# Performance work log

Hardware: AMD Instinct MI355X
Metric: run time of the kernel (lower is better)

Reference implementation:

```python
import jax, jax.numpy as jnp
import numpy as np

N_NODES = 50000
N_EDGES = 1600000
IN_DIM, HID_DIM, OUT_DIM, HEADS = 128, 128, 64, 8
NEG_SLOPE = 0.2
BN_EPS = 1e-5


def setup_inputs() -> dict:
    key = jax.random.key(0)
    ks = jax.random.split(key, 12)
    hpc = HID_DIM // HEADS  # per-head channels of layer 1
    return {
        "x": jax.random.normal(ks[0], (N_NODES, IN_DIM), jnp.float32),
        "edge_index": jax.random.randint(ks[1], (2, N_EDGES), 0, N_NODES, jnp.int64),
        "W1": jax.random.normal(ks[2], (IN_DIM, HEADS * hpc), jnp.float32) * 0.05,
        "a1_src": jax.random.normal(ks[3], (HEADS, hpc), jnp.float32) * 0.1,
        "a1_dst": jax.random.normal(ks[4], (HEADS, hpc), jnp.float32) * 0.1,
        "b1": jnp.zeros((HEADS * hpc,), jnp.float32),
        "bn_gamma": jnp.ones((HID_DIM,), jnp.float32),
        "bn_beta": jnp.zeros((HID_DIM,), jnp.float32),
        "W2": jax.random.normal(ks[5], (HID_DIM, OUT_DIM), jnp.float32) * 0.05,
        "a2_src": jax.random.normal(ks[6], (1, OUT_DIM), jnp.float32) * 0.1,
        "a2_dst": jax.random.normal(ks[7], (1, OUT_DIM), jnp.float32) * 0.1,
        "b2": jnp.zeros((OUT_DIM,), jnp.float32),
    }


def _gat_conv(x, src, dst, W, a_src, a_dst, bias, heads, n_nodes):
    # x: [N, Fin]; src/dst: [E'] (self-loops already appended)
    hpc = W.shape[1] // heads
    h = (x @ W).reshape(n_nodes, heads, hpc)                 # [N,H,C]
    alpha_s = jnp.einsum("nhc,hc->nh", h, a_src)             # [N,H]
    alpha_d = jnp.einsum("nhc,hc->nh", h, a_dst)
    e = alpha_s[src] + alpha_d[dst]                          # [E',H]
    e = jax.nn.leaky_relu(e, NEG_SLOPE)
    # segment softmax over destination neighborhoods
    m = jax.ops.segment_max(e, dst, num_segments=n_nodes)    # [N,H]
    m = jnp.where(jnp.isfinite(m), m, 0.0)
    ee = jnp.exp(e - m[dst])
    denom = jax.ops.segment_sum(ee, dst, num_segments=n_nodes)
    alpha = ee / (denom[dst] + 1e-16)                        # [E',H]
    msg = h[src] * alpha[:, :, None]                         # [E',H,C]
    out = jax.ops.segment_sum(msg, dst, num_segments=n_nodes)  # [N,H,C]
    return out.reshape(n_nodes, heads * hpc) + bias


def _batch_norm(x, gamma, beta):
    mu = jnp.mean(x, axis=0)
    var = jnp.var(x, axis=0)
    return gamma * (x - mu) * jax.lax.rsqrt(var + BN_EPS) + beta


def reference(x, edge_index, W1, a1_src, a1_dst, b1, bn_gamma, bn_beta, W2, a2_src, a2_dst, b2):
    n = x.shape[0]
    loops = jnp.arange(n, dtype=edge_index.dtype)
    src = jnp.concatenate([edge_index[0], loops])            # PyG add_self_loops
    dst = jnp.concatenate([edge_index[1], loops])
    h = _gat_conv(x, src, dst, W1, a1_src, a1_dst, b1, HEADS, n)
    h = _batch_norm(h, bn_gamma, bn_beta)
    h = jax.nn.elu(h)
    # dropout: identity at inference
    out = _gat_conv(h, src, dst, W2, a2_src, a2_dst, b2, 1, n)
    return out
```

## Files before the change

### kernel.cpp

```cpp
#include <hip/hip_runtime.h>
#include <hip/hip_bf16.h>

#define N_NODES 50000
#define N_EDGES 1600000
#define HEADS 8
#define NBK 196
#define NBLK 196

typedef unsigned short u16;
typedef unsigned int u32;

__device__ __forceinline__ float bf2f(u16 u) {
  union { u32 i; float f; } v; v.i = ((u32)u) << 16; return v.f;
}
__device__ __forceinline__ float bflo(u32 p) {
  union { u32 i; float f; } v; v.i = p << 16; return v.f;
}
__device__ __forceinline__ float bfhi(u32 p) {
  union { u32 i; float f; } v; v.i = p & 0xffff0000u; return v.f;
}
__device__ __forceinline__ u16 f2bf(float f) {
  union { float f; u32 i; } v; v.f = f;
  u32 r = v.i + 0x7fff + ((v.i >> 16) & 1);
  return (u16)(r >> 16);
}
__device__ __forceinline__ u32 pack2(float a, float b) {
  return (u32)f2bf(a) | ((u32)f2bf(b) << 16);
}

__global__ void k_detect(const u16* __restrict__ x, const u32* __restrict__ ei,
                         int* __restrict__ flags) {
  __shared__ int cbig, cnz;
  if (threadIdx.x == 0) { cbig = 0; cnz = 0; }
  __syncthreads();
  int lb = 0, ln = 0;
  for (int i = threadIdx.x; i < 4096; i += 256) {
    int ex = (x[i] >> 7) & 0xff;
    lb += (ex >= 140);
    if (i < 2048) ln += (ei[2 * i + 1] != 0);
  }
  atomicAdd(&cbig, lb); atomicAdd(&cnz, ln);
  __syncthreads();
  if (threadIdx.x == 0) {
    flags[0] = (cbig > 16) ? 1 : 0;
    flags[1] = (cnz == 0) ? 1 : 0;
  }
}

__global__ void k_convsmall(const void* a1s, const void* a1d, const void* b1,
                            const void* gam, const void* bet, const void* a2s,
                            const void* a2d, const void* b2, const void* W1,
                            const void* W2, float* __restrict__ outbuf,
                            const int* __restrict__ flags) {
  int i = blockIdx.x * 256 + threadIdx.x;
  if (i >= 25408) return;
  const void* src; int off;
  if (i >= 17216)      { src = W2;  off = i - 17216; }
  else if (i >= 832)   { src = W1;  off = i - 832; }
  else if (i >= 768)   { src = b2;  off = i - 768; }
  else if (i >= 704)   { src = a2d; off = i - 704; }
  else if (i >= 640)   { src = a2s; off = i - 640; }
  else if (i >= 512)   { src = bet; off = i - 512; }
  else if (i >= 384)   { src = gam; off = i - 384; }
  else if (i >= 256)   { src = b1;  off = i - 256; }
  else if (i >= 128)   { src = a1d; off = i - 128; }
  else                 { src = a1s; off = i; }
  outbuf[i] = flags[0] ? ((const float*)src)[off] : bf2f(((const u16*)src)[off]);
}

__global__ __launch_bounds__(256) void k_hist(const int* __restrict__ ei,
                                              int* __restrict__ H,
                                              int* __restrict__ totals,
                                              const int* __restrict__ flags) {
  __shared__ int hist[NBK];
  int t = threadIdx.x, blk = blockIdx.x;
  for (int i = t; i < NBK; i += 256) hist[i] = 0;
  __syncthreads();
  bool i64 = flags[1] != 0;
  int base = blk * 8192;
  for (int k = 0; k < 32; k++) {
    int e = base + k * 256 + t;
    if (e < N_EDGES) {
      int d = i64 ? ei[2 * (N_EDGES + e)] : ei[N_EDGES + e];
      atomicAdd(&hist[d >> 8], 1);
    }
  }
  __syncthreads();
  for (int i = t; i < NBK; i += 256) {
    H[i * NBLK + blk] = hist[i];
    atomicAdd(&totals[i], hist[i]);
  }
}

__global__ void k_scan_tot(const int* __restrict__ totals, int* __restrict__ bucketBase) {
  __shared__ int tmp[256];
  int t = threadIdx.x;
  int v = (t < NBK) ? totals[t] : 0;
  tmp[t] = v; __syncthreads();
  for (int o = 1; o < 256; o <<= 1) {
    int x = (t >= o) ? tmp[t - o] : 0; __syncthreads();
    tmp[t] += x; __syncthreads();
  }
  if (t < NBK) bucketBase[t] = tmp[t] - v;
  if (t == NBK - 1) bucketBase[NBK] = tmp[t];
}

__global__ void k_scan_blk(const int* __restrict__ H, const int* __restrict__ bucketBase,
                           int* __restrict__ P) {
  __shared__ int tmp[256];
  int t = threadIdx.x, b = blockIdx.x;
  int v = (t < NBLK) ? H[b * NBLK + t] : 0;
  tmp[t] = v; __syncthreads();
  for (int o = 1; o < 256; o <<= 1) {
    int x = (t >= o) ? tmp[t - o] : 0; __syncthreads();
    tmp[t] += x; __syncthreads();
  }
  if (t < NBLK) P[b * NBLK + t] = bucketBase[b] + tmp[t] - v;
}

__global__ __launch_bounds__(256) void k_bucket(const int* __restrict__ ei,
                                                const int* __restrict__ P,
                                                u32* __restrict__ buf,
                                                const int* __restrict__ flags) {
  __shared__ int cur[NBK];
  int t = threadIdx.x, blk = blockIdx.x;
  for (int i = t; i < NBK; i += 256) cur[i] = P[i * NBLK + blk];
  __syncthreads();
  bool i64 = flags[1] != 0;
  int base = blk * 8192;
  for (int k = 0; k < 32; k++) {
    int e = base + k * 256 + t;
    if (e < N_EDGES) {
      int s = i64 ? ei[2 * e] : ei[e];
      int d = i64 ? ei[2 * (N_EDGES + e)] : ei[N_EDGES + e];
      int pos = atomicAdd(&cur[d >> 8], 1);
      buf[pos] = ((u32)(d & 255) << 16) | (u32)s;
    }
  }
}

__global__ __launch_bounds__(256) void k_csr(const u32* __restrict__ buf,
                                             const int* __restrict__ bucketBase,
                                             int* __restrict__ row_start,
                                             int* __restrict__ deg,
                                             int* __restrict__ csr, int N) {
  __shared__ int cnt[256], scn[256], cur[256];
  int b = blockIdx.x, t = threadIdx.x;
  int lo = bucketBase[b], hi = bucketBase[b + 1];
  cnt[t] = 0; __syncthreads();
  for (int e = lo + t; e < hi; e += 256) atomicAdd(&cnt[(buf[e] >> 16) & 255], 1);
  __syncthreads();
  int v = cnt[t];
  scn[t] = v; __syncthreads();
  for (int o = 1; o < 256; o <<= 1) {
    int x = (t >= o) ? scn[t - o] : 0; __syncthreads();
    scn[t] += x; __syncthreads();
  }
  int excl = scn[t] - v;
  int node = b * 256 + t;
  if (node < N) { row_start[node] = lo + excl; deg[node] = v; }
  cur[t] = lo + excl;
  __syncthreads();
  for (int e = lo + t; e < hi; e += 256) {
    u32 p = buf[e];
    int d8 = (p >> 16) & 255;
    int pos = atomicAdd(&cur[d8], 1);
    csr[pos] = p & 0xffff;
  }
}

template <bool EPI, bool AFLAG>
__global__ __launch_bounds__(256) void k_gemm(const void* __restrict__ A,
                                              const float* __restrict__ B,
                                              const float* __restrict__ scale,
                                              const float* __restrict__ shift,
                                              u16* __restrict__ C, int M, int ncoltot,
                                              const int* __restrict__ flags) {
  constexpr int K = 128, KP = K + 4;
  __shared__ float As[64 * KP];
  __shared__ float Bs[K * 64];
  int t = threadIdx.x;
  int row0 = blockIdx.x * 64, co = blockIdx.y * 64;
  bool af32 = AFLAG ? (flags[0] != 0) : false;
  for (int i = t; i < K * 16; i += 256) {
    int r = i >> 4, c4 = i & 15;
    ((float4*)Bs)[r * 16 + c4] = ((const float4*)B)[(size_t)r * (ncoltot >> 2) + (co >> 2) + c4];
  }
  for (int i = t; i < 64 * 32; i += 256) {
    int r = i >> 5, c4 = i & 31;
    float4 v = make_float4(0.f, 0.f, 0.f, 0.f);
    int row = row0 + r;
    if (row < M) {
      if (af32) {
        v = ((const float4*)A)[(size_t)row * 32 + c4];
      } else {
        uint2 p = ((const uint2*)A)[(size_t)row * 32 + c4];
        v.x = bflo(p.x); v.y = bfhi(p.x); v.z = bflo(p.y); v.w = bfhi(p.y);
      }
      if (EPI) {
        int c = c4 * 4;
        v.x = fmaf(v.x, scale[c],     shift[c]);     v.x = v.x > 0.f ? v.x : __expf(v.x) - 1.f;
        v.y = fmaf(v.y, scale[c + 1], shift[c + 1]); v.y = v.y > 0.f ? v.y : __expf(v.y) - 1.f;
        v.z = fmaf(v.z, scale[c + 2], shift[c + 2]); v.z = v.z > 0.f ? v.z : __expf(v.z) - 1.f;
        v.w = fmaf(v.w, scale[c + 3], shift[c + 3]); v.w = v.w > 0.f ? v.w : __expf(v.w) - 1.f;
      }
    }
    *(float4*)&As[r * KP + c4 * 4] = v;
  }
  __syncthreads();
  int tx = t & 7, ty = t >> 3;
  int c0 = tx * 8, r0 = ty * 2;
  float acc[2][8];
#pragma unroll
  for (int i = 0; i < 2; i++) for (int j = 0; j < 8; j++) acc[i][j] = 0.f;
#pragma unroll 4
  for (int k = 0; k < K; k++) {
    float4 b0 = *(const float4*)&Bs[k * 64 + c0];
    float4 b1 = *(const float4*)&Bs[k * 64 + c0 + 4];
    float a0 = As[r0 * KP + k];
    float a1 = As[(r0 + 1) * KP + k];
    acc[0][0] = fmaf(a0, b0.x, acc[0][0]); acc[0][1] = fmaf(a0, b0.y, acc[0][1]);
    acc[0][2] = fmaf(a0, b0.z, acc[0][2]); acc[0][3] = fmaf(a0, b0.w, acc[0][3]);
    acc[0][4] = fmaf(a0, b1.x, acc[0][4]); acc[0][5] = fmaf(a0, b1.y, acc[0][5]);
    acc[0][6] = fmaf(a0, b1.z, acc[0][6]); acc[0][7] = fmaf(a0, b1.w, acc[0][7]);
    acc[1][0] = fmaf(a1, b0.x, acc[1][0]); acc[1][1] = fmaf(a1, b0.y, acc[1][1]);
    acc[1][2] = fmaf(a1, b0.z, acc[1][2]); acc[1][3] = fmaf(a1, b0.w, acc[1][3]);
    acc[1][4] = fmaf(a1, b1.x, acc[1][4]); acc[1][5] = fmaf(a1, b1.y, acc[1][5]);
    acc[1][6] = fmaf(a1, b1.z, acc[1][6]); acc[1][7] = fmaf(a1, b1.w, acc[1][7]);
  }
#pragma unroll
  for (int i = 0; i < 2; i++) {
    int row = row0 + r0 + i;
    if (row < M) {
      u32* cp = (u32*)&C[(size_t)row * ncoltot + co + c0];
      cp[0] = pack2(acc[i][0], acc[i][1]);
      cp[1] = pack2(acc[i][2], acc[i][3]);
      cp[2] = pack2(acc[i][4], acc[i][5]);
      cp[3] = pack2(acc[i][6], acc[i][7]);
    }
  }
}

__global__ void k_alpha1(const u16* __restrict__ h1b, const float* __restrict__ a1s,
                         const float* __restrict__ a1d, float* __restrict__ as_out,
                         float* __restrict__ ad_out, int N) {
  int idx = blockIdx.x * 256 + threadIdx.x;
  if (idx >= N * HEADS) return;
  int n = idx >> 3, h = idx & 7;
  const u32* hp = (const u32*)&h1b[((size_t)n << 7) + (h << 4)];
  float s = 0.f, d = 0.f;
#pragma unroll
  for (int q = 0; q < 8; q++) {
    u32 p = hp[q];
    float v0 = bflo(p), v1 = bfhi(p);
    int b = (h << 4) + q * 2;
    s = fmaf(v0, a1s[b], s); s = fmaf(v1, a1s[b + 1], s);
    d = fmaf(v0, a1d[b], d); d = fmaf(v1, a1d[b + 1], d);
  }
  as_out[idx] = s; ad_out[idx] = d;
}

__global__ __launch_bounds__(256) void k_agg1(const u16* __restrict__ h1b,
                                              const float* __restrict__ as_,
                                              const float* __restrict__ ad_,
                                              const int* __restrict__ csr,
                                              const int* __restrict__ row_start,
                                              const int* __restrict__ deg,
                                              const float* __restrict__ b1,
                                              u16* __restrict__ out, int N) {
  int w = threadIdx.x >> 6;
  int node = blockIdx.x * 4 + w;
  if (node >= N) return;
  int l = threadIdx.x & 63;
  int head = l >> 3;
  int st = row_start[node], cnt = deg[node];
  float ad = ad_[(node << 3) | head];
  float s = 0.f, a0 = 0.f, a1 = 0.f;
  const u32* h32 = (const u32*)h1b;
  int j = 0;
  for (; j + 4 <= cnt; j += 4) {
    int s0 = csr[st + j], s1 = csr[st + j + 1], s2 = csr[st + j + 2], s3 = csr[st + j + 3];
    float e0 = as_[(s0 << 3) | head], e1 = as_[(s1 << 3) | head];
    float e2 = as_[(s2 << 3) | head], e3 = as_[(s3 << 3) | head];
    u32 h0 = h32[(s0 << 6) | l], h1v = h32[(s1 << 6) | l];
    u32 h2v = h32[(s2 << 6) | l], h3 = h32[(s3 << 6) | l];
    e0 += ad; e0 = fmaxf(e0, 0.2f * e0); float p0 = __expf(e0);
    e1 += ad; e1 = fmaxf(e1, 0.2f * e1); float p1 = __expf(e1);
    e2 += ad; e2 = fmaxf(e2, 0.2f * e2); float p2 = __expf(e2);
    e3 += ad; e3 = fmaxf(e3, 0.2f * e3); float p3 = __expf(e3);
    s += (p0 + p1) + (p2 + p3);
    a0 = fmaf(p0, bflo(h0), a0);  a1 = fmaf(p0, bfhi(h0), a1);
    a0 = fmaf(p1, bflo(h1v), a0); a1 = fmaf(p1, bfhi(h1v), a1);
    a0 = fmaf(p2, bflo(h2v), a0); a1 = fmaf(p2, bfhi(h2v), a1);
    a0 = fmaf(p3, bflo(h3), a0);  a1 = fmaf(p3, bfhi(h3), a1);
  }
  for (; j < cnt; j++) {
    int s0 = csr[st + j];
    float e0 = as_[(s0 << 3) | head] + ad;
    e0 = fmaxf(e0, 0.2f * e0);
    float p0 = __expf(e0);
    u32 h0 = h32[(s0 << 6) | l];
    s += p0;
    a0 = fmaf(p0, bflo(h0), a0); a1 = fmaf(p0, bfhi(h0), a1);
  }
  {
    float e0 = as_[(node << 3) | head] + ad;
    e0 = fmaxf(e0, 0.2f * e0);
    float p0 = __expf(e0);
    u32 h0 = h32[((size_t)node << 6) | l];
    s += p0;
    a0 = fmaf(p0, bflo(h0), a0); a1 = fmaf(p0, bfhi(h0), a1);
  }
  float inv = 1.f / (s + 1e-16f);
  int c0 = l * 2;
  ((u32*)out)[((size_t)node << 6) + l] =
      pack2(fmaf(a0, inv, b1[c0]), fmaf(a1, inv, b1[c0 + 1]));
}

__global__ void k_bnstat(const u16* __restrict__ h, float* __restrict__ gsum,
                         float* __restrict__ gsq, int N) {
  __shared__ float ts[256], tq[256];
  int t = threadIdx.x, col = t & 127, rr = t >> 7;
  int row0 = blockIdx.x * 128;
  float s = 0.f, q = 0.f;
  for (int r = rr; r < 128; r += 2) {
    int row = row0 + r;
    if (row < N) {
      float v = bf2f(h[((size_t)row << 7) + col]);
      s += v; q = fmaf(v, v, q);
    }
  }
  ts[t] = s; tq[t] = q; __syncthreads();
  if (t < 128) {
    atomicAdd(&gsum[t], ts[t] + ts[t + 128]);
    atomicAdd(&gsq[t], tq[t] + tq[t + 128]);
  }
}

__global__ void k_bnfin(const float* __restrict__ gsum, const float* __restrict__ gsq,
                        const float* __restrict__ gamma, const float* __restrict__ beta,
                        float* __restrict__ scale, float* __restrict__ shift, int N) {
  int t = threadIdx.x;
  if (t >= 128) return;
  float mu = gsum[t] / (float)N;
  float var = fmaxf(gsq[t] / (float)N - mu * mu, 0.f);
  float s = gamma[t] * rsqrtf(var + 1e-5f);
  scale[t] = s;
  shift[t] = beta[t] - mu * s;
}

__global__ void k_alpha2(const u16* __restrict__ h2b, const float* __restrict__ a2s,
                         const float* __restrict__ a2d, float* __restrict__ as_out,
                         float* __restrict__ ad_out, int N) {
  int w = threadIdx.x >> 6;
  int node = blockIdx.x * 4 + w;
  if (node >= N) return;
  int l = threadIdx.x & 63;
  float v = bf2f(h2b[((size_t)node << 6) + l]);
  float vs = v * a2s[l], vd = v * a2d[l];
  for (int o = 32; o; o >>= 1) { vs += __shfl_xor(vs, o, 64); vd += __shfl_xor(vd, o, 64); }
  if (l == 0) { as_out[node] = vs; ad_out[node] = vd; }
}

__global__ __launch_bounds__(256) void k_agg2(const u16* __restrict__ h2b,
                                              const float* __restrict__ as_,
                                              const float* __restrict__ ad_,
                                              const int* __restrict__ csr,
                                              const int* __restrict__ row_start,
                                              const int* __restrict__ deg,
                                              const float* __restrict__ b2,
                                              void* __restrict__ out,
                                              const int* __restrict__ flags, int N) {
  int w = threadIdx.x >> 6;
  int node = blockIdx.x * 4 + w;
  if (node >= N) return;
  int l = threadIdx.x & 63;
  int st = row_start[node], cnt = deg[node];
  float ad = ad_[node];
  float s = 0.f, a = 0.f;
  int j = 0;
  for (; j + 4 <= cnt; j += 4) {
    int s0 = csr[st + j], s1 = csr[st + j + 1], s2 = csr[st + j + 2], s3 = csr[st + j + 3];
    float e0 = as_[s0], e1 = as_[s1], e2 = as_[s2], e3 = as_[s3];
    u16 v0 = h2b[(s0 << 6) | l], v1 = h2b[(s1 << 6) | l];
    u16 v2 = h2b[(s2 << 6) | l], v3 = h2b[(s3 << 6) | l];
    e0 += ad; e0 = fmaxf(e0, 0.2f * e0); float p0 = __expf(e0);
    e1 += ad; e1 = fmaxf(e1, 0.2f * e1); float p1 = __expf(e1);
    e2 += ad; e2 = fmaxf(e2, 0.2f * e2); float p2 = __expf(e2);
    e3 += ad; e3 = fmaxf(e3, 0.2f * e3); float p3 = __expf(e3);
    s += (p0 + p1) + (p2 + p3);
    a = fmaf(p0, bf2f(v0), a); a = fmaf(p1, bf2f(v1), a);
    a = fmaf(p2, bf2f(v2), a); a = fmaf(p3, bf2f(v3), a);
  }
  for (; j < cnt; j++) {
    int s0 = csr[st + j];
    float e0 = as_[s0] + ad;
    e0 = fmaxf(e0, 0.2f * e0);
    float p0 = __expf(e0);
    s += p0;
    a = fmaf(p0, bf2f(h2b[(s0 << 6) | l]), a);
  }
  {
    float e0 = as_[node] + ad;
    e0 = fmaxf(e0, 0.2f * e0);
    float p0 = __expf(e0);
    s += p0;
    a = fmaf(p0, bf2f(h2b[((size_t)node << 6) | l]), a);
  }
  float r = a / (s + 1e-16f) + b2[l];
  size_t idx = ((size_t)node << 6) + l;
  if (flags[0]) ((float*)out)[idx] = r;
  else          ((u16*)out)[idx] = f2bf(r);
}

extern "C" void kernel_launch(void* const* d_in, const int* in_sizes, int n_in,
                              void* d_out, int out_size, void* d_ws, size_t ws_size,
                              hipStream_t stream) {
  const void* x   = d_in[0];
  const int*  ei  = (const int*)d_in[1];
  const void* W1  = d_in[2];
  const void* a1s = d_in[3];
  const void* a1d = d_in[4];
  const void* b1  = d_in[5];
  const void* gam = d_in[6];
  const void* bet = d_in[7];
  const void* W2  = d_in[8];
  const void* a2s = d_in[9];
  const void* a2d = d_in[10];
  const void* b2  = d_in[11];

  char* ws = (char*)d_ws;
  size_t off = 0;
  auto alloc = [&](size_t bytes) -> void* {
    void* p = ws + off;
    off += (bytes + 255) & ~(size_t)255;
    return p;
  };
  int* flags = (int*)alloc(256);
  char* zreg = (char*)alloc(2048);
  int* totals = (int*)zreg;
  float* gsum = (float*)(zreg + 1024);
  float* gsq  = gsum + 128;
  int* H  = (int*)alloc((size_t)NBK * NBLK * 4);
  int* P  = (int*)alloc((size_t)NBK * NBLK * 4);
  int* bucketBase = (int*)alloc(1024);
  u32* ebuf = (u32*)alloc((size_t)N_EDGES * 4);
  int* csr = (int*)alloc((size_t)N_EDGES * 4);
  int* row_start = (int*)alloc((size_t)N_NODES * 4);
  int* deg = (int*)alloc((size_t)N_NODES * 4);
  float* smallf = (float*)alloc(25408 * 4);
  float* a1sf = smallf;        float* a1df = smallf + 128;
  float* b1f  = smallf + 256;  float* gamf = smallf + 384;
  float* betf = smallf + 512;  float* a2sf = smallf + 640;
  float* a2df = smallf + 704;  float* b2f  = smallf + 768;
  float* W1f  = smallf + 832;  float* W2f  = smallf + 17216;
  u16* h1b  = (u16*)alloc((size_t)N_NODES * 128 * 2);
  u16* h1ob = (u16*)alloc((size_t)N_NODES * 128 * 2);
  u16* h2b  = (u16*)alloc((size_t)N_NODES * 64 * 2);
  float* al1s = (float*)alloc((size_t)N_NODES * 8 * 4);
  float* al1d = (float*)alloc((size_t)N_NODES * 8 * 4);
  float* scale = (float*)alloc(512);
  float* shift = (float*)alloc(512);
  float* al2s = (float*)alloc((size_t)N_NODES * 4);
  float* al2d = (float*)alloc((size_t)N_NODES * 4);
  if (off > ws_size) return;

  hipMemsetAsync(zreg, 0, 2048, stream);
  k_detect<<<1, 256, 0, stream>>>((const u16*)x, (const u32*)ei, flags);
  k_convsmall<<<100, 256, 0, stream>>>(a1s, a1d, b1, gam, bet, a2s, a2d, b2, W1, W2,
                                       smallf, flags);

  k_hist<<<NBLK, 256, 0, stream>>>(ei, H, totals, flags);
  k_scan_tot<<<1, 256, 0, stream>>>(totals, bucketBase);
  k_scan_blk<<<NBK, 256, 0, stream>>>(H, bucketBase, P);
  k_bucket<<<NBLK, 256, 0, stream>>>(ei, P, ebuf, flags);
  k_csr<<<NBK, 256, 0, stream>>>(ebuf, bucketBase, row_start, deg, csr, N_NODES);

  dim3 g1((N_NODES + 63) / 64, 2);
  k_gemm<false, true><<<g1, 256, 0, stream>>>(x, W1f, nullptr, nullptr, h1b,
                                              N_NODES, 128, flags);
  k_alpha1<<<(N_NODES * HEADS + 255) / 256, 256, 0, stream>>>(h1b, a1sf, a1df,
                                                              al1s, al1d, N_NODES);
  k_agg1<<<(N_NODES + 3) / 4, 256, 0, stream>>>(h1b, al1s, al1d, csr, row_start, deg,
                                                b1f, h1ob, N_NODES);

  k_bnstat<<<(N_NODES + 127) / 128, 256, 0, stream>>>(h1ob, gsum, gsq, N_NODES);
  k_bnfin<<<1, 128, 0, stream>>>(gsum, gsq, gamf, betf, scale, shift, N_NODES);

  dim3 g2((N_NODES + 63) / 64, 1);
  k_gemm<true, false><<<g2, 256, 0, stream>>>(h1ob, W2f, scale, shift, h2b,
                                              N_NODES, 64, flags);
  k_alpha2<<<(N_NODES + 3) / 4, 256, 0, stream>>>(h2b, a2sf, a2df, al2s, al2d, N_NODES);
  k_agg2<<<(N_NODES + 3) / 4, 256, 0, stream>>>(h2b, al2s, al2d, csr, row_start, deg,
                                                b2f, d_out, flags, N_NODES);
}
```

Measured before the change: 400.9 us.

## Replace FP32 SIMT GEMMs with bf16 MFMA kernels and pre-transposed weights

Both dense projections now run on bf16 MFMA 16x16x32 instructions instead of scalar FP32 FMAs. The weight-conversion kernel now writes transposed bf16 weight copies so B tiles load as contiguous K-vectors. The first GEMM covers all 128 output columns in one block, and inputs are rounded to bf16 before the multiply, which costs some precision. The aggregation kernels also use readfirstlane to keep node, row start and degree in scalar registers.

```diff
diff --git a/kernel.cpp b/kernel.cpp
--- a/kernel.cpp
+++ b/kernel.cpp
@@ -9,6 +9,8 @@
 
 typedef unsigned short u16;
 typedef unsigned int u32;
+typedef __attribute__((ext_vector_type(8))) short bf16x8;
+typedef __attribute__((ext_vector_type(4))) float f32x4;
 
 __device__ __forceinline__ float bf2f(u16 u) {
   union { u32 i; float f; } v; v.i = ((u32)u) << 16; return v.f;
@@ -50,22 +52,33 @@
 __global__ void k_convsmall(const void* a1s, const void* a1d, const void* b1,
                             const void* gam, const void* bet, const void* a2s,
                             const void* a2d, const void* b2, const void* W1,
-                            const void* W2, float* __restrict__ outbuf,
+                            const void* W2, float* __restrict__ smallf,
+                            u16* __restrict__ w1t, u16* __restrict__ w2t,
                             const int* __restrict__ flags) {
   int i = blockIdx.x * 256 + threadIdx.x;
   if (i >= 25408) return;
-  const void* src; int off;
-  if (i >= 17216)      { src = W2;  off = i - 17216; }
-  else if (i >= 832)   { src = W1;  off = i - 832; }
-  else if (i >= 768)   { src = b2;  off = i - 768; }
-  else if (i >= 704)   { src = a2d; off = i - 704; }
-  else if (i >= 640)   { src = a2s; off = i - 640; }
-  else if (i >= 512)   { src = bet; off = i - 512; }
-  else if (i >= 384)   { src = gam; off = i - 384; }
-  else if (i >= 256)   { src = b1;  off = i - 256; }
-  else if (i >= 128)   { src = a1d; off = i - 128; }
-  else                 { src = a1s; off = i; }
-  outbuf[i] = flags[0] ? ((const float*)src)[off] : bf2f(((const u16*)src)[off]);
+  bool f32 = flags[0] != 0;
+  auto ld = [&](const void* p, int off) -> float {
+    return f32 ? ((const float*)p)[off] : bf2f(((const u16*)p)[off]);
+  };
+  if (i >= 17216) {
+    int j = i - 17216, n = j >> 7, k = j & 127;
+    w2t[j] = f2bf(ld(W2, k * 64 + n));
+  } else if (i >= 832) {
+    int j = i - 832, n = j >> 7, k = j & 127;
+    w1t[j] = f2bf(ld(W1, k * 128 + n));
+  } else {
+    const void* src; int off;
+    if (i >= 768)      { src = b2;  off = i - 768; }
+    else if (i >= 704) { src = a2d; off = i - 704; }
+    else if (i >= 640) { src = a2s; off = i - 640; }
+    else if (i >= 512) { src = bet; off = i - 512; }
+    else if (i >= 384) { src = gam; off = i - 384; }
+    else if (i >= 256) { src = b1;  off = i - 256; }
+    else if (i >= 128) { src = a1d; off = i - 128; }
+    else               { src = a1s; off = i; }
+    smallf[i] = ld(src, off);
+  }
 }
 
 __global__ __launch_bounds__(256) void k_hist(const int* __restrict__ ei,
@@ -163,80 +176,78 @@
   __syncthreads();
   for (int e = lo + t; e < hi; e += 256) {
     u32 p = buf[e];
-    int d8 = (p >> 16) & 255;
-    int pos = atomicAdd(&cur[d8], 1);
+    int pos = atomicAdd(&cur[(p >> 16) & 255], 1);
     csr[pos] = p & 0xffff;
   }
 }
 
-template <bool EPI, bool AFLAG>
-__global__ __launch_bounds__(256) void k_gemm(const void* __restrict__ A,
-                                              const float* __restrict__ B,
-                                              const float* __restrict__ scale,
-                                              const float* __restrict__ shift,
-                                              u16* __restrict__ C, int M, int ncoltot,
-                                              const int* __restrict__ flags) {
-  constexpr int K = 128, KP = K + 4;
-  __shared__ float As[64 * KP];
-  __shared__ float Bs[K * 64];
+template <int NCOLS, bool EPI, bool AFLAG>
+__global__ __launch_bounds__(256) void k_gemm_mfma(const void* __restrict__ A,
+                                                   const u16* __restrict__ BT,
+                                                   const float* __restrict__ scale,
+                                                   const float* __restrict__ shift,
+                                                   u16* __restrict__ C, int M,
+                                                   const int* __restrict__ flags) {
+  constexpr int KP = 136;
+  constexpr int NT = NCOLS / 16;
+  __shared__ u16 As[64 * KP];
+  __shared__ u16 Bs[NCOLS * KP];
   int t = threadIdx.x;
-  int row0 = blockIdx.x * 64, co = blockIdx.y * 64;
+  int row0 = blockIdx.x * 64;
   bool af32 = AFLAG ? (flags[0] != 0) : false;
-  for (int i = t; i < K * 16; i += 256) {
-    int r = i >> 4, c4 = i & 15;
-    ((float4*)Bs)[r * 16 + c4] = ((const float4*)B)[(size_t)r * (ncoltot >> 2) + (co >> 2) + c4];
+
+  for (int i = t; i < NCOLS * 16; i += 256) {
+    int n = i >> 4, q = i & 15;
+    *(uint4*)&Bs[n * KP + q * 8] = ((const uint4*)BT)[n * 16 + q];
   }
   for (int i = t; i < 64 * 32; i += 256) {
     int r = i >> 5, c4 = i & 31;
-    float4 v = make_float4(0.f, 0.f, 0.f, 0.f);
     int row = row0 + r;
+    uint2 pk = make_uint2(0u, 0u);
     if (row < M) {
-      if (af32) {
-        v = ((const float4*)A)[(size_t)row * 32 + c4];
+      if (EPI) {
+        uint2 p = ((const uint2*)A)[(size_t)row * 32 + c4];
+        int c = c4 * 4;
+        float v0 = bflo(p.x), v1 = bfhi(p.x), v2 = bflo(p.y), v3 = bfhi(p.y);
+        v0 = fmaf(v0, scale[c],     shift[c]);     v0 = v0 > 0.f ? v0 : __expf(v0) - 1.f;
+        v1 = fmaf(v1, scale[c + 1], shift[c + 1]); v1 = v1 > 0.f ? v1 : __expf(v1) - 1.f;
+        v2 = fmaf(v2, scale[c + 2], shift[c + 2]); v2 = v2 > 0.f ? v2 : __expf(v2) - 1.f;
+        v3 = fmaf(v3, scale[c + 3], shift[c + 3]); v3 = v3 > 0.f ? v3 : __expf(v3) - 1.f;
+        pk.x = pack2(v0, v1); pk.y = pack2(v2, v3);
+      } else if (af32) {
+        float4 v = ((const float4*)A)[(size_t)row * 32 + c4];
+        pk.x = pack2(v.x, v.y); pk.y = pack2(v.z, v.w);
       } else {
-        uint2 p = ((const uint2*)A)[(size_t)row * 32 + c4];
-        v.x = bflo(p.x); v.y = bfhi(p.x); v.z = bflo(p.y); v.w = bfhi(p.y);
-      }
-      if (EPI) {
-        int c = c4 * 4;
-        v.x = fmaf(v.x, scale[c],     shift[c]);     v.x = v.x > 0.f ? v.x : __expf(v.x) - 1.f;
-        v.y = fmaf(v.y, scale[c + 1], shift[c + 1]); v.y = v.y > 0.f ? v.y : __expf(v.y) - 1.f;
-        v.z = fmaf(v.z, scale[c + 2], shift[c + 2]); v.z = v.z > 0.f ? v.z : __expf(v.z) - 1.f;
-        v.w = fmaf(v.w, scale[c + 3], shift[c + 3]); v.w = v.w > 0.f ? v.w : __expf(v.w) - 1.f;
+        pk = ((const uint2*)A)[(size_t)row * 32 + c4];
       }
     }
-    *(float4*)&As[r * KP + c4 * 4] = v;
-  }
-  __syncthreads();
-  int tx = t & 7, ty = t >> 3;
-  int c0 = tx * 8, r0 = ty * 2;
-  float acc[2][8];
+    *(uint2*)&As[r * KP + c4 * 4] = pk;
+  }
+  __syncthreads();
+
+  int lane = t & 63, w = t >> 6;
+  int m = lane & 15, quad = lane >> 4;
+  f32x4 acc[NT];
 #pragma unroll
-  for (int i = 0; i < 2; i++) for (int j = 0; j < 8; j++) acc[i][j] = 0.f;
-#pragma unroll 4
-  for (int k = 0; k < K; k++) {
-    float4 b0 = *(const float4*)&Bs[k * 64 + c0];
-    float4 b1 = *(const float4*)&Bs[k * 64 + c0 + 4];
-    float a0 = As[r0 * KP + k];
-    float a1 = As[(r0 + 1) * KP + k];
-    acc[0][0] = fmaf(a0, b0.x, acc[0][0]); acc[0][1] = fmaf(a0, b0.y, acc[0][1]);
-    acc[0][2] = fmaf(a0, b0.z, acc[0][2]); acc[0][3] = fmaf(a0, b0.w, acc[0][3]);
-    acc[0][4] = fmaf(a0, b1.x, acc[0][4]); acc[0][5] = fmaf(a0, b1.y, acc[0][5]);
-    acc[0][6] = fmaf(a0, b1.z, acc[0][6]); acc[0][7] = fmaf(a0, b1.w, acc[0][7]);
-    acc[1][0] = fmaf(a1, b0.x, acc[1][0]); acc[1][1] = fmaf(a1, b0.y, acc[1][1]);
-    acc[1][2] = fmaf(a1, b0.z, acc[1][2]); acc[1][3] = fmaf(a1, b0.w, acc[1][3]);
-    acc[1][4] = fmaf(a1, b1.x, acc[1][4]); acc[1][5] = fmaf(a1, b1.y, acc[1][5]);
-    acc[1][6] = fmaf(a1, b1.z, acc[1][6]); acc[1][7] = fmaf(a1, b1.w, acc[1][7]);
-  }
+  for (int nt = 0; nt < NT; nt++) acc[nt] = (f32x4)(0.f);
+  const u16* aBase = &As[(w * 16 + m) * KP + quad * 8];
+  const u16* bBase = &Bs[m * KP + quad * 8];
 #pragma unroll
-  for (int i = 0; i < 2; i++) {
-    int row = row0 + r0 + i;
-    if (row < M) {
-      u32* cp = (u32*)&C[(size_t)row * ncoltot + co + c0];
-      cp[0] = pack2(acc[i][0], acc[i][1]);
-      cp[1] = pack2(acc[i][2], acc[i][3]);
-      cp[2] = pack2(acc[i][4], acc[i][5]);
-      cp[3] = pack2(acc[i][6], acc[i][7]);
+  for (int ks = 0; ks < 4; ks++) {
+    bf16x8 af = *(const bf16x8*)(aBase + ks * 32);
+#pragma unroll
+    for (int nt = 0; nt < NT; nt++) {
+      bf16x8 bf = *(const bf16x8*)(bBase + nt * 16 * KP + ks * 32);
+      acc[nt] = __builtin_amdgcn_mfma_f32_16x16x32_bf16(af, bf, acc[nt], 0, 0, 0);
+    }
+  }
+  int orow0 = row0 + w * 16 + quad * 4;
+#pragma unroll
+  for (int nt = 0; nt < NT; nt++) {
+#pragma unroll
+    for (int r = 0; r < 4; r++) {
+      int row = orow0 + r;
+      if (row < M) C[(size_t)row * NCOLS + nt * 16 + m] = f2bf(acc[nt][r]);
     }
   }
 }
@@ -268,22 +279,24 @@
                                               const int* __restrict__ deg,
                                               const float* __restrict__ b1,
                                               u16* __restrict__ out, int N) {
-  int w = threadIdx.x >> 6;
-  int node = blockIdx.x * 4 + w;
+  int node = blockIdx.x * 4 + (threadIdx.x >> 6);
   if (node >= N) return;
   int l = threadIdx.x & 63;
   int head = l >> 3;
-  int st = row_start[node], cnt = deg[node];
-  float ad = ad_[(node << 3) | head];
+  int node_u = __builtin_amdgcn_readfirstlane(node);
+  int st = __builtin_amdgcn_readfirstlane(row_start[node_u]);
+  int cnt = __builtin_amdgcn_readfirstlane(deg[node_u]);
+  const int* cp = csr + st;
+  const u32* h32 = (const u32*)h1b;
+  float ad = ad_[(node_u << 3) | head];
   float s = 0.f, a0 = 0.f, a1 = 0.f;
-  const u32* h32 = (const u32*)h1b;
   int j = 0;
   for (; j + 4 <= cnt; j += 4) {
-    int s0 = csr[st + j], s1 = csr[st + j + 1], s2 = csr[st + j + 2], s3 = csr[st + j + 3];
-    float e0 = as_[(s0 << 3) | head], e1 = as_[(s1 << 3) | head];
-    float e2 = as_[(s2 << 3) | head], e3 = as_[(s3 << 3) | head];
-    u32 h0 = h32[(s0 << 6) | l], h1v = h32[(s1 << 6) | l];
-    u32 h2v = h32[(s2 << 6) | l], h3 = h32[(s3 << 6) | l];
+    int s0 = cp[j], s1 = cp[j + 1], s2 = cp[j + 2], s3 = cp[j + 3];
+    float e0 = (as_ + (s0 << 3))[head], e1 = (as_ + (s1 << 3))[head];
+    float e2 = (as_ + (s2 << 3))[head], e3 = (as_ + (s3 << 3))[head];
+    u32 h0 = (h32 + (s0 << 6))[l], h1v = (h32 + (s1 << 6))[l];
+    u32 h2v = (h32 + (s2 << 6))[l], h3 = (h32 + (s3 << 6))[l];
     e0 += ad; e0 = fmaxf(e0, 0.2f * e0); float p0 = __expf(e0);
     e1 += ad; e1 = fmaxf(e1, 0.2f * e1); float p1 = __expf(e1);
     e2 += ad; e2 = fmaxf(e2, 0.2f * e2); float p2 = __expf(e2);
@@ -295,25 +308,25 @@
     a0 = fmaf(p3, bflo(h3), a0);  a1 = fmaf(p3, bfhi(h3), a1);
   }
   for (; j < cnt; j++) {
-    int s0 = csr[st + j];
-    float e0 = as_[(s0 << 3) | head] + ad;
+    int s0 = cp[j];
+    float e0 = (as_ + (s0 << 3))[head] + ad;
     e0 = fmaxf(e0, 0.2f * e0);
     float p0 = __expf(e0);
-    u32 h0 = h32[(s0 << 6) | l];
+    u32 h0 = (h32 + (s0 << 6))[l];
     s += p0;
     a0 = fmaf(p0, bflo(h0), a0); a1 = fmaf(p0, bfhi(h0), a1);
   }
   {
-    float e0 = as_[(node << 3) | head] + ad;
+    float e0 = (as_ + (node_u << 3))[head] + ad;
     e0 = fmaxf(e0, 0.2f * e0);
     float p0 = __expf(e0);
-    u32 h0 = h32[((size_t)node << 6) | l];
+    u32 h0 = (h32 + (node_u << 6))[l];
     s += p0;
     a0 = fmaf(p0, bflo(h0), a0); a1 = fmaf(p0, bfhi(h0), a1);
   }
   float inv = 1.f / (s + 1e-16f);
   int c0 = l * 2;
-  ((u32*)out)[((size_t)node << 6) + l] =
+  ((u32*)out)[((size_t)node_u << 6) + l] =
       pack2(fmaf(a0, inv, b1[c0]), fmaf(a1, inv, b1[c0 + 1]));
 }
 
@@ -371,19 +384,21 @@
                                               const float* __restrict__ b2,
                                               void* __restrict__ out,
                                               const int* __restrict__ flags, int N) {
-  int w = threadIdx.x >> 6;
-  int node = blockIdx.x * 4 + w;
+  int node = blockIdx.x * 4 + (threadIdx.x >> 6);
   if (node >= N) return;
   int l = threadIdx.x & 63;
-  int st = row_start[node], cnt = deg[node];
-  float ad = ad_[node];
+  int node_u = __builtin_amdgcn_readfirstlane(node);
+  int st = __builtin_amdgcn_readfirstlane(row_start[node_u]);
+  int cnt = __builtin_amdgcn_readfirstlane(deg[node_u]);
+  const int* cp = csr + st;
+  float ad = ad_[node_u];
   float s = 0.f, a = 0.f;
   int j = 0;
   for (; j + 4 <= cnt; j += 4) {
-    int s0 = csr[st + j], s1 = csr[st + j + 1], s2 = csr[st + j + 2], s3 = csr[st + j + 3];
+    int s0 = cp[j], s1 = cp[j + 1], s2 = cp[j + 2], s3 = cp[j + 3];
     float e0 = as_[s0], e1 = as_[s1], e2 = as_[s2], e3 = as_[s3];
-    u16 v0 = h2b[(s0 << 6) | l], v1 = h2b[(s1 << 6) | l];
-    u16 v2 = h2b[(s2 << 6) | l], v3 = h2b[(s3 << 6) | l];
+    u16 v0 = (h2b + (s0 << 6))[l], v1 = (h2b + (s1 << 6))[l];
+    u16 v2 = (h2b + (s2 << 6))[l], v3 = (h2b + (s3 << 6))[l];
     e0 += ad; e0 = fmaxf(e0, 0.2f * e0); float p0 = __expf(e0);
     e1 += ad; e1 = fmaxf(e1, 0.2f * e1); float p1 = __expf(e1);
     e2 += ad; e2 = fmaxf(e2, 0.2f * e2); float p2 = __expf(e2);
@@ -393,22 +408,22 @@
     a = fmaf(p2, bf2f(v2), a); a = fmaf(p3, bf2f(v3), a);
   }
   for (; j < cnt; j++) {
-    int s0 = csr[st + j];
+    int s0 = cp[j];
     float e0 = as_[s0] + ad;
     e0 = fmaxf(e0, 0.2f * e0);
     float p0 = __expf(e0);
     s += p0;
-    a = fmaf(p0, bf2f(h2b[(s0 << 6) | l]), a);
+    a = fmaf(p0, bf2f((h2b + (s0 << 6))[l]), a);
   }
   {
-    float e0 = as_[node] + ad;
+    float e0 = as_[node_u] + ad;
     e0 = fmaxf(e0, 0.2f * e0);
     float p0 = __expf(e0);
     s += p0;
-    a = fmaf(p0, bf2f(h2b[((size_t)node << 6) | l]), a);
+    a = fmaf(p0, bf2f((h2b + (node_u << 6))[l]), a);
   }
   float r = a / (s + 1e-16f) + b2[l];
-  size_t idx = ((size_t)node << 6) + l;
+  size_t idx = ((size_t)node_u << 6) + l;
   if (flags[0]) ((float*)out)[idx] = r;
   else          ((u16*)out)[idx] = f2bf(r);
 }
@@ -448,12 +463,13 @@
   int* csr = (int*)alloc((size_t)N_EDGES * 4);
   int* row_start = (int*)alloc((size_t)N_NODES * 4);
   int* deg = (int*)alloc((size_t)N_NODES * 4);
-  float* smallf = (float*)alloc(25408 * 4);
+  float* smallf = (float*)alloc(832 * 4);
   float* a1sf = smallf;        float* a1df = smallf + 128;
   float* b1f  = smallf + 256;  float* gamf = smallf + 384;
   float* betf = smallf + 512;  float* a2sf = smallf + 640;
   float* a2df = smallf + 704;  float* b2f  = smallf + 768;
-  float* W1f  = smallf + 832;  float* W2f  = smallf + 17216;
+  u16* w1t = (u16*)alloc(16384 * 2);
+  u16* w2t = (u16*)alloc(8192 * 2);
   u16* h1b  = (u16*)alloc((size_t)N_NODES * 128 * 2);
   u16* h1ob = (u16*)alloc((size_t)N_NODES * 128 * 2);
   u16* h2b  = (u16*)alloc((size_t)N_NODES * 64 * 2);
@@ -468,7 +484,7 @@
   hipMemsetAsync(zreg, 0, 2048, stream);
   k_detect<<<1, 256, 0, stream>>>((const u16*)x, (const u32*)ei, flags);
   k_convsmall<<<100, 256, 0, stream>>>(a1s, a1d, b1, gam, bet, a2s, a2d, b2, W1, W2,
-                                       smallf, flags);
+                                       smallf, w1t, w2t, flags);
 
   k_hist<<<NBLK, 256, 0, stream>>>(ei, H, totals, flags);
   k_scan_tot<<<1, 256, 0, stream>>>(totals, bucketBase);
@@ -476,9 +492,8 @@
   k_bucket<<<NBLK, 256, 0, stream>>>(ei, P, ebuf, flags);
   k_csr<<<NBK, 256, 0, stream>>>(ebuf, bucketBase, row_start, deg, csr, N_NODES);
 
-  dim3 g1((N_NODES + 63) / 64, 2);
-  k_gemm<false, true><<<g1, 256, 0, stream>>>(x, W1f, nullptr, nullptr, h1b,
-                                              N_NODES, 128, flags);
+  k_gemm_mfma<128, false, true><<<(N_NODES + 63) / 64, 256, 0, stream>>>(
+      x, w1t, nullptr, nullptr, h1b, N_NODES, flags);
   k_alpha1<<<(N_NODES * HEADS + 255) / 256, 256, 0, stream>>>(h1b, a1sf, a1df,
                                                               al1s, al1d, N_NODES);
   k_agg1<<<(N_NODES + 3) / 4, 256, 0, stream>>>(h1b, al1s, al1d, csr, row_start, deg,
@@ -487,9 +502,8 @@
   k_bnstat<<<(N_NODES + 127) / 128, 256, 0, stream>>>(h1ob, gsum, gsq, N_NODES);
   k_bnfin<<<1, 128, 0, stream>>>(gsum, gsq, gamf, betf, scale, shift, N_NODES);
 
-  dim3 g2((N_NODES + 63) / 64, 1);
-  k_gemm<true, false><<<g2, 256, 0, stream>>>(h1ob, W2f, scale, shift, h2b,
-                                              N_NODES, 64, flags);
+  k_gemm_mfma<64, true, false><<<(N_NODES + 63) / 64, 256, 0, stream>>>(
+      h1ob, w2t, scale, shift, h2b, N_NODES, flags);
   k_alpha2<<<(N_NODES + 3) / 4, 256, 0, stream>>>(h2b, a2sf, a2df, al2s, al2d, N_NODES);
   k_agg2<<<(N_NODES + 3) / 4, 256, 0, stream>>>(h2b, al2s, al2d, csr, row_start, deg,
                                                 b2f, d_out, flags, N_NODES);
```

After: 350.0 us. -12.7%, faster.
